# Kernel tuning notes

Measured on AMD Instinct MI355X. Metric: run time of the kernel, lower is better.

The kernel has to match this reference:

```python
import jax, jax.numpy as jnp
import numpy as np

DIM, DEPTH, HEADS, DIM_HEAD, MLP_DIM = 512, 6, 8, 64, 2048
INNER = HEADS * DIM_HEAD
EPS = 1e-5


def _layernorm(x, s, b):
    mu = jnp.mean(x, axis=-1, keepdims=True)
    var = jnp.mean(jnp.square(x - mu), axis=-1, keepdims=True)
    return (x - mu) * jax.lax.rsqrt(var + EPS) * s + b


def setup_inputs() -> dict:
    key = jax.random.key(0)
    ks = jax.random.split(key, 12)
    d = {
        "x": jax.random.normal(ks[0], (8, 1024, DIM), dtype=jnp.float32),
        "ln1_s": jnp.ones((DEPTH, DIM), jnp.float32),
        "ln1_b": jnp.zeros((DEPTH, DIM), jnp.float32),
        "w_qkv": jax.random.normal(ks[1], (DEPTH, DIM, 3 * INNER), dtype=jnp.float32) * (DIM ** -0.5),
        "w_out": jax.random.normal(ks[2], (DEPTH, INNER, DIM), dtype=jnp.float32) * (INNER ** -0.5),
        "b_out": jnp.zeros((DEPTH, DIM), jnp.float32),
        "ln2_s": jnp.ones((DEPTH, DIM), jnp.float32),
        "ln2_b": jnp.zeros((DEPTH, DIM), jnp.float32),
        "w1": jax.random.normal(ks[3], (DEPTH, DIM, MLP_DIM), dtype=jnp.float32) * (DIM ** -0.5),
        "b1": jnp.zeros((DEPTH, MLP_DIM), jnp.float32),
        "w2": jax.random.normal(ks[4], (DEPTH, MLP_DIM, DIM), dtype=jnp.float32) * (MLP_DIM ** -0.5),
        "b2": jnp.zeros((DEPTH, DIM), jnp.float32),
    }
    return d


def reference(x, ln1_s, ln1_b, w_qkv, w_out, b_out, ln2_s, ln2_b, w1, b1, w2, b2):
    b, n, _ = x.shape
    scale = DIM_HEAD ** -0.5
    for i in range(DEPTH):
        # --- PreNorm Attention with residual ---
        h = _layernorm(x, ln1_s[i], ln1_b[i])
        qkv = h @ w_qkv[i]                                  # [b, n, 3*inner]
        q, k, v = jnp.split(qkv, 3, axis=-1)
        q = q.reshape(b, n, HEADS, DIM_HEAD)
        k = k.reshape(b, n, HEADS, DIM_HEAD)
        v = v.reshape(b, n, HEADS, DIM_HEAD)
        dots = jnp.einsum('bihd,bjhd->bhij', q, k) * scale  # [b, h, n, n]
        attn = jax.nn.softmax(dots, axis=-1)
        out = jnp.einsum('bhij,bjhd->bihd', attn, v).reshape(b, n, INNER)
        x = out @ w_out[i] + b_out[i] + x
        # --- PreNorm FeedForward with residual ---
        h = _layernorm(x, ln2_s[i], ln2_b[i])
        h = jax.nn.gelu(h @ w1[i] + b1[i], approximate=False)
        x = h @ w2[i] + b2[i] + x
    return x
```

## Files before the change

kernel.cpp:

```cpp
#include <hip/hip_runtime.h>
#include <cstdint>
#include <cstddef>

#define M_TOK 8192
#define DIMM  512
#define HEADS 8
#define DH    64
#define MLPD  2048
#define DEPTH 6

typedef unsigned short u16;
typedef unsigned int   u32;
typedef __attribute__((ext_vector_type(8))) short short8;
typedef __attribute__((ext_vector_type(4))) float f32x4;

__device__ __forceinline__ float bf2f(u16 u){ return __uint_as_float(((u32)u) << 16); }
__device__ __forceinline__ u16 f2bf(float f){
    u32 x = __float_as_uint(f);
    u32 r = x + 0x7fffu + ((x >> 16) & 1u);
    return (u16)(r >> 16);
}
__device__ __forceinline__ u32 cvt_pk_bf16(float a, float b){
    u32 r;
    asm("v_cvt_pk_bf16_f32 %0, %1, %2" : "=v"(r) : "v"(a), "v"(b));
    return r;
}
__device__ __forceinline__ void async16(const u16* g, u16* l){
    __builtin_amdgcn_global_load_lds(
        (const __attribute__((address_space(1))) void*)(uintptr_t)(const void*)g,
        (__attribute__((address_space(3))) void*)(u32)(uintptr_t)(void*)l,
        16, 0, 0);
}
__device__ __forceinline__ void xcd_swizzle(int& bx, int& by){
    int nbx = gridDim.x, nby = gridDim.y;
    if ((nby & 7) == 0){
        int i = by * nbx + bx;
        int xcd = i & 7, j = i >> 3, ypg = nby >> 3;
        int yq = j / nbx;
        by = xcd * ypg + yq;
        bx = j - yq * nbx;
    }
}

__global__ void k_transpose_cvt(const float* __restrict__ in, u16* __restrict__ out, int R, int C){
    __shared__ u16 tile[32][33];
    size_t zoff = (size_t)blockIdx.z * R * C;
    in += zoff; out += zoff;
    int c0 = blockIdx.x * 32, r0 = blockIdx.y * 32;
    int tx = threadIdx.x, ty = threadIdx.y;
    #pragma unroll
    for (int i = 0; i < 32; i += 8)
        tile[ty + i][tx] = f2bf(in[(size_t)(r0 + ty + i) * C + c0 + tx]);
    __syncthreads();
    #pragma unroll
    for (int i = 0; i < 32; i += 8)
        out[(size_t)(c0 + ty + i) * R + r0 + tx] = tile[tx][ty + i];
}

__global__ __launch_bounds__(256) void k_layernorm(const float* __restrict__ x,
                                                   const float* __restrict__ s,
                                                   const float* __restrict__ b,
                                                   u16* __restrict__ out){
    int row = blockIdx.x * 4 + (threadIdx.x >> 6);
    int lane = threadIdx.x & 63;
    const float* xp = x + (size_t)row * DIMM + lane * 8;
    float v[8];
    #pragma unroll
    for (int c = 0; c < 8; c++) v[c] = xp[c];
    float sum = 0.f, sq = 0.f;
    #pragma unroll
    for (int c = 0; c < 8; c++){ sum += v[c]; sq += v[c] * v[c]; }
    #pragma unroll
    for (int m = 32; m >= 1; m >>= 1){
        sum += __shfl_xor(sum, m);
        sq  += __shfl_xor(sq,  m);
    }
    float mu  = sum * (1.f / DIMM);
    float var = sq * (1.f / DIMM) - mu * mu;
    float rs  = rsqrtf(var + 1e-5f);
    u16* op = out + (size_t)row * DIMM + lane * 8;
    #pragma unroll
    for (int c = 0; c < 8; c++){
        int col = lane * 8 + c;
        op[c] = f2bf((v[c] - mu) * rs * s[col] + b[col]);
    }
}

__device__ __forceinline__ float gelu_exact(float v){
    return 0.5f * v * (1.f + erff(v * 0.70710678118654752f));
}

#define LDT64 72

template<int MODE>
__global__ __launch_bounds__(256) void k_gemm128b(const u16* __restrict__ A,
                                                  const u16* __restrict__ Bt,
                                                  const float* __restrict__ bias,
                                                  u16* __restrict__ Cout,
                                                  int M, int N, int K){
    __shared__ u16 As[2][128 * 64];
    __shared__ u16 Bs[2][128 * 64];
    int bx = blockIdx.x, by = blockIdx.y;
    xcd_swizzle(bx, by);
    int m0 = by * 128, n0 = bx * 128;
    int t = threadIdx.x;
    int w = t >> 6, lane = t & 63;
    int mi = lane & 15, quad = lane >> 4;
    int wr = w >> 1, wc = w & 1;

    int grow = lane >> 3, gcol = (lane & 7) * 8;
    const u16* agl = A  + (size_t)(m0 + w * 32 + grow) * K + gcol;
    const u16* bgl = Bt + (size_t)(n0 + w * 32 + grow) * K + gcol;

    f32x4 acc[4][4];
    #pragma unroll
    for (int mt = 0; mt < 4; mt++)
        #pragma unroll
        for (int nt = 0; nt < 4; nt++) acc[mt][nt] = (f32x4){0.f, 0.f, 0.f, 0.f};

    int nt_k = K >> 6;
    {
        u16* asl = &As[0][(w * 32) * 64];
        u16* bsl = &Bs[0][(w * 32) * 64];
        #pragma unroll
        for (int i = 0; i < 4; i++){
            async16(agl + (size_t)(i * 8) * K, asl + i * 8 * 64);
            async16(bgl + (size_t)(i * 8) * K, bsl + i * 8 * 64);
        }
    }
    __syncthreads();

    for (int td = 0; td < nt_k; td++){
        int cur = td & 1;
        if (td + 1 < nt_k){
            int k0 = (td + 1) << 6;
            u16* asl = &As[cur ^ 1][(w * 32) * 64];
            u16* bsl = &Bs[cur ^ 1][(w * 32) * 64];
            #pragma unroll
            for (int i = 0; i < 4; i++){
                async16(agl + (size_t)(i * 8) * K + k0, asl + i * 8 * 64);
                async16(bgl + (size_t)(i * 8) * K + k0, bsl + i * 8 * 64);
            }
        }
        const u16* Ab = &As[cur][0];
        const u16* Bb = &Bs[cur][0];
        #pragma unroll
        for (int kk = 0; kk < 64; kk += 32){
            short8 af[4], bf[4];
            #pragma unroll
            for (int mt = 0; mt < 4; mt++)
                af[mt] = *(const short8*)&Ab[(wr * 64 + mt * 16 + mi) * 64 + kk + quad * 8];
            #pragma unroll
            for (int nt = 0; nt < 4; nt++)
                bf[nt] = *(const short8*)&Bb[(wc * 64 + nt * 16 + mi) * 64 + kk + quad * 8];
            #pragma unroll
            for (int mt = 0; mt < 4; mt++)
                #pragma unroll
                for (int nt = 0; nt < 4; nt++)
                    acc[mt][nt] = __builtin_amdgcn_mfma_f32_16x16x32_bf16(af[mt], bf[nt], acc[mt][nt], 0, 0, 0);
        }
        __syncthreads();
    }

    float bv[4];
    if (MODE == 1){
        #pragma unroll
        for (int nt = 0; nt < 4; nt++) bv[nt] = bias[n0 + wc * 64 + nt * 16 + mi];
    }
    u16* cs = ((u16*)As) + w * 16 * LDT64;
    int erow = lane >> 2, ecol = (lane & 3) * 16;
    #pragma unroll
    for (int mt = 0; mt < 4; mt++){
        #pragma unroll
        for (int nt = 0; nt < 4; nt++)
            #pragma unroll
            for (int r = 0; r < 4; r++){
                float v = acc[mt][nt][r];
                if (MODE == 1) v = gelu_exact(v + bv[nt]);
                cs[(quad * 4 + r) * LDT64 + nt * 16 + mi] = f2bf(v);
            }
        uint4 c0 = *(const uint4*)&cs[erow * LDT64 + ecol];
        uint4 c1 = *(const uint4*)&cs[erow * LDT64 + ecol + 8];
        u16* cp = Cout + (size_t)(m0 + wr * 64 + mt * 16 + erow) * N + n0 + wc * 64 + ecol;
        *(uint4*)cp       = c0;
        *(uint4*)(cp + 8) = c1;
    }
}

__global__ __launch_bounds__(256) void k_gemm128_res(const u16* __restrict__ A,
                                                     const u16* __restrict__ Bt,
                                                     const float* __restrict__ bias,
                                                     float* __restrict__ xres,
                                                     int M, int N, int K){
    __shared__ u16 As[2][128 * 64];
    __shared__ u16 Bs[2][128 * 64];
    int bx = blockIdx.x, by = blockIdx.y;
    xcd_swizzle(bx, by);
    int m0 = by * 128, n0 = bx * 128;
    int t = threadIdx.x;
    int w = t >> 6, lane = t & 63;
    int mi = lane & 15, quad = lane >> 4;
    int wr = w >> 1, wc = w & 1;

    int grow = lane >> 3, gcol = (lane & 7) * 8;
    const u16* agl = A  + (size_t)(m0 + w * 32 + grow) * K + gcol;
    const u16* bgl = Bt + (size_t)(n0 + w * 32 + grow) * K + gcol;

    f32x4 acc[4][4];
    #pragma unroll
    for (int mt = 0; mt < 4; mt++)
        #pragma unroll
        for (int nt = 0; nt < 4; nt++) acc[mt][nt] = (f32x4){0.f, 0.f, 0.f, 0.f};

    int nt_k = K >> 6;
    {
        u16* asl = &As[0][(w * 32) * 64];
        u16* bsl = &Bs[0][(w * 32) * 64];
        #pragma unroll
        for (int i = 0; i < 4; i++){
            async16(agl + (size_t)(i * 8) * K, asl + i * 8 * 64);
            async16(bgl + (size_t)(i * 8) * K, bsl + i * 8 * 64);
        }
    }
    __syncthreads();

    for (int td = 0; td < nt_k; td++){
        int cur = td & 1;
        if (td + 1 < nt_k){
            int k0 = (td + 1) << 6;
            u16* asl = &As[cur ^ 1][(w * 32) * 64];
            u16* bsl = &Bs[cur ^ 1][(w * 32) * 64];
            #pragma unroll
            for (int i = 0; i < 4; i++){
                async16(agl + (size_t)(i * 8) * K + k0, asl + i * 8 * 64);
                async16(bgl + (size_t)(i * 8) * K + k0, bsl + i * 8 * 64);
            }
        }
        const u16* Ab = &As[cur][0];
        const u16* Bb = &Bs[cur][0];
        #pragma unroll
        for (int kk = 0; kk < 64; kk += 32){
            short8 af[4], bf[4];
            #pragma unroll
            for (int mt = 0; mt < 4; mt++)
                af[mt] = *(const short8*)&Ab[(wr * 64 + mt * 16 + mi) * 64 + kk + quad * 8];
            #pragma unroll
            for (int nt = 0; nt < 4; nt++)
                bf[nt] = *(const short8*)&Bb[(wc * 64 + nt * 16 + mi) * 64 + kk + quad * 8];
            #pragma unroll
            for (int mt = 0; mt < 4; mt++)
                #pragma unroll
                for (int nt = 0; nt < 4; nt++)
                    acc[mt][nt] = __builtin_amdgcn_mfma_f32_16x16x32_bf16(af[mt], bf[nt], acc[mt][nt], 0, 0, 0);
        }
        __syncthreads();
    }

    float bv[4];
    #pragma unroll
    for (int nt = 0; nt < 4; nt++) bv[nt] = bias[n0 + wc * 64 + nt * 16 + mi];
    float* cs = ((float*)As) + w * 16 * LDT64;
    int erow = lane >> 2, ecol = (lane & 3) * 16;
    #pragma unroll
    for (int mt = 0; mt < 4; mt++){
        #pragma unroll
        for (int nt = 0; nt < 4; nt++)
            #pragma unroll
            for (int r = 0; r < 4; r++)
                cs[(quad * 4 + r) * LDT64 + nt * 16 + mi] = acc[mt][nt][r] + bv[nt];
        float* xp = xres + (size_t)(m0 + wr * 64 + mt * 16 + erow) * N + n0 + wc * 64 + ecol;
        #pragma unroll
        for (int j = 0; j < 4; j++){
            float4 cv = *(const float4*)&cs[erow * LDT64 + ecol + j * 4];
            float4 xv = *(const float4*)(xp + j * 4);
            xv.x += cv.x; xv.y += cv.y; xv.z += cv.z; xv.w += cv.w;
            *(float4*)(xp + j * 4) = xv;
        }
    }
}

#define LDK 72
#define C1_LOG2E 0.18033688011112042f
#define C2_LOG2E 11.541560327111707f

__global__ __launch_bounds__(256) void k_flash(const u16* __restrict__ qkv, u16* __restrict__ out){
    __shared__ u16 Ks[64 * LDK];
    __shared__ u16 Vt[80 * LDK];
    __shared__ u16 Ps[4][32 * LDK];
    int wg = (blockIdx.x & 7) * 64 + (blockIdx.x >> 3);
    int qt = wg & 7, h = (wg >> 3) & 7, b = wg >> 6;
    int t = threadIdx.x;
    int w = t >> 6, lane = t & 63;
    int mi = lane & 15, quad = lane >> 4;

    for (int i = t; i < 16 * 64; i += 256){
        int d = i >> 6, kk = i & 63;
        Vt[(64 + d) * LDK + kk] = 0x3F80;
    }

    const u16* base = qkv + ((size_t)b * 1024) * 1536;
    int hoff = h * 64;

    short8 qf[2][2];
    #pragma unroll
    for (int qh = 0; qh < 2; qh++){
        int qrow = qt * 128 + w * 32 + qh * 16 + mi;
        const u16* qp = base + (size_t)qrow * 1536 + hoff + quad * 8;
        qf[qh][0] = *(const short8*)(qp);
        qf[qh][1] = *(const short8*)(qp + 32);
    }

    f32x4 o[2][4];
    f32x4 lacc[2];
    #pragma unroll
    for (int qh = 0; qh < 2; qh++){
        #pragma unroll
        for (int nb = 0; nb < 4; nb++) o[qh][nb] = (f32x4){0.f, 0.f, 0.f, 0.f};
        lacc[qh] = (f32x4){0.f, 0.f, 0.f, 0.f};
    }

    int kkey = t >> 2, kseg = t & 3;
    const u16* kgp = base + (size_t)kkey * 1536 + 512 + hoff + kseg * 16;
    int vkey = lane, vdg = w;
    const u16* vgp = base + (size_t)vkey * 1536 + 1024 + hoff + vdg * 16;

    uint4 kv0 = *(const uint4*)(kgp);
    uint4 kv1 = *(const uint4*)(kgp + 8);
    uint4 vv0 = *(const uint4*)(vgp);
    uint4 vv1 = *(const uint4*)(vgp + 8);

    for (int kt = 0; kt < 16; kt++){
        __syncthreads();
        *(uint4*)&Ks[kkey * LDK + kseg * 16]     = kv0;
        *(uint4*)&Ks[kkey * LDK + kseg * 16 + 8] = kv1;
        u16 vtmp[16];
        *(uint4*)&vtmp[0] = vv0;
        *(uint4*)&vtmp[8] = vv1;
        #pragma unroll
        for (int i = 0; i < 16; i++)
            Vt[(vdg * 16 + i) * LDK + vkey] = vtmp[i];
        __syncthreads();

        if (kt < 15){
            size_t koff = (size_t)(kt + 1) * 64 * 1536;
            kv0 = *(const uint4*)(kgp + koff);
            kv1 = *(const uint4*)(kgp + koff + 8);
            vv0 = *(const uint4*)(vgp + koff);
            vv1 = *(const uint4*)(vgp + koff + 8);
        }

        short8 kb[4][2];
        #pragma unroll
        for (int nb = 0; nb < 4; nb++){
            kb[nb][0] = *(const short8*)&Ks[(nb * 16 + mi) * LDK + quad * 8];
            kb[nb][1] = *(const short8*)&Ks[(nb * 16 + mi) * LDK + quad * 8 + 32];
        }
        #pragma unroll
        for (int qh = 0; qh < 2; qh++){
            #pragma unroll
            for (int nb = 0; nb < 4; nb++){
                f32x4 z = (f32x4){0.f, 0.f, 0.f, 0.f};
                z = __builtin_amdgcn_mfma_f32_16x16x32_bf16(qf[qh][0], kb[nb][0], z, 0, 0, 0);
                z = __builtin_amdgcn_mfma_f32_16x16x32_bf16(qf[qh][1], kb[nb][1], z, 0, 0, 0);
                float e0 = exp2f(fmaf(z[0], C1_LOG2E, -C2_LOG2E));
                float e1 = exp2f(fmaf(z[1], C1_LOG2E, -C2_LOG2E));
                float e2 = exp2f(fmaf(z[2], C1_LOG2E, -C2_LOG2E));
                float e3 = exp2f(fmaf(z[3], C1_LOG2E, -C2_LOG2E));
                u32 p01 = cvt_pk_bf16(e0, e1);
                u32 p23 = cvt_pk_bf16(e2, e3);
                u16* pp = &Ps[w][(qh * 16 + quad * 4) * LDK + nb * 16 + mi];
                pp[0]       = (u16)p01;
                pp[LDK]     = (u16)(p01 >> 16);
                pp[2 * LDK] = (u16)p23;
                pp[3 * LDK] = (u16)(p23 >> 16);
            }
        }
        short8 vb[4][2], lb[2];
        #pragma unroll
        for (int nb = 0; nb < 4; nb++){
            vb[nb][0] = *(const short8*)&Vt[(nb * 16 + mi) * LDK + quad * 8];
            vb[nb][1] = *(const short8*)&Vt[(nb * 16 + mi) * LDK + quad * 8 + 32];
        }
        lb[0] = *(const short8*)&Vt[(64 + mi) * LDK + quad * 8];
        lb[1] = *(const short8*)&Vt[(64 + mi) * LDK + quad * 8 + 32];
        #pragma unroll
        for (int qh = 0; qh < 2; qh++){
            const short8 a0 = *(const short8*)&Ps[w][(qh * 16 + mi) * LDK + quad * 8];
            const short8 a1 = *(const short8*)&Ps[w][(qh * 16 + mi) * LDK + quad * 8 + 32];
            #pragma unroll
            for (int nb = 0; nb < 4; nb++){
                o[qh][nb] = __builtin_amdgcn_mfma_f32_16x16x32_bf16(a0, vb[nb][0], o[qh][nb], 0, 0, 0);
                o[qh][nb] = __builtin_amdgcn_mfma_f32_16x16x32_bf16(a1, vb[nb][1], o[qh][nb], 0, 0, 0);
            }
            lacc[qh] = __builtin_amdgcn_mfma_f32_16x16x32_bf16(a0, lb[0], lacc[qh], 0, 0, 0);
            lacc[qh] = __builtin_amdgcn_mfma_f32_16x16x32_bf16(a1, lb[1], lacc[qh], 0, 0, 0);
        }
    }
    #pragma unroll
    for (int qh = 0; qh < 2; qh++){
        float invl[4];
        #pragma unroll
        for (int r = 0; r < 4; r++) invl[r] = 1.f / lacc[qh][r];
        u16* op = out + ((size_t)b * 1024 + qt * 128 + w * 32 + qh * 16) * 512 + hoff;
        #pragma unroll
        for (int nb = 0; nb < 4; nb++){
            u32 c01 = cvt_pk_bf16(o[qh][nb][0] * invl[0], o[qh][nb][1] * invl[1]);
            u32 c23 = cvt_pk_bf16(o[qh][nb][2] * invl[2], o[qh][nb][3] * invl[3]);
            u16* cp = op + (size_t)(quad * 4) * 512 + nb * 16 + mi;
            cp[0]       = (u16)c01;
            cp[512]     = (u16)(c01 >> 16);
            cp[2 * 512] = (u16)c23;
            cp[3 * 512] = (u16)(c23 >> 16);
        }
    }
}

extern "C" void kernel_launch(void* const* d_in, const int* in_sizes, int n_in,
                              void* d_out, int out_size, void* d_ws, size_t ws_size,
                              hipStream_t stream){
    const float* x_in  = (const float*)d_in[0];
    const float* ln1_s = (const float*)d_in[1];
    const float* ln1_b = (const float*)d_in[2];
    const float* w_qkv = (const float*)d_in[3];
    const float* w_out = (const float*)d_in[4];
    const float* b_out = (const float*)d_in[5];
    const float* ln2_s = (const float*)d_in[6];
    const float* ln2_b = (const float*)d_in[7];
    const float* w1    = (const float*)d_in[8];
    const float* b1    = (const float*)d_in[9];
    const float* w2    = (const float*)d_in[10];
    const float* b2    = (const float*)d_in[11];
    float* out = (float*)d_out;

    char* ws = (char*)d_ws;
    float* x_f32 = (float*)ws;   ws += (size_t)M_TOK * DIMM * 4;
    u16* bufA    = (u16*)ws;     ws += (size_t)M_TOK * DIMM * 2;
    u16* bufB    = (u16*)ws;     ws += (size_t)M_TOK * MLPD * 2;
    u16* wbase   = (u16*)ws;
    size_t per_layer_w = (size_t)(1536 + 512 + 2048 + 2048) * 512;

    size_t used_big = (size_t)(ws - (char*)d_ws) + per_layer_w * 2 * DEPTH;
    bool big = (ws_size >= used_big);

    u16* ln_out   = bufA;
    u16* attn_out = bufA;
    u16* qkv      = bufB;
    u16* mlp_h    = bufB;

    size_t x_bytes = (size_t)M_TOK * DIMM * sizeof(float);
    hipMemcpyAsync(x_f32, x_in, x_bytes, hipMemcpyDeviceToDevice, stream);

    const size_t off_qkv = 0;
    const size_t off_out = (size_t)1536 * 512;
    const size_t off_w1  = off_out + (size_t)512 * 512;
    const size_t off_w2  = off_w1 + (size_t)2048 * 512;

    if (big){
        k_transpose_cvt<<<dim3(48, 16, 6), dim3(32, 8), 0, stream>>>(w_qkv, wbase + off_qkv * DEPTH, 512, 1536);
        k_transpose_cvt<<<dim3(16, 16, 6), dim3(32, 8), 0, stream>>>(w_out, wbase + off_out * DEPTH, 512, 512);
        k_transpose_cvt<<<dim3(64, 16, 6), dim3(32, 8), 0, stream>>>(w1,    wbase + off_w1  * DEPTH, 512, 2048);
        k_transpose_cvt<<<dim3(16, 64, 6), dim3(32, 8), 0, stream>>>(w2,    wbase + off_w2  * DEPTH, 2048, 512);
    }

    for (int i = 0; i < DEPTH; i++){
        u16 *wqkvT, *woutT, *w1T, *w2T;
        if (big){
            wqkvT = wbase + off_qkv * DEPTH + (size_t)i * 1536 * 512;
            woutT = wbase + off_out * DEPTH + (size_t)i * 512 * 512;
            w1T   = wbase + off_w1  * DEPTH + (size_t)i * 2048 * 512;
            w2T   = wbase + off_w2  * DEPTH + (size_t)i * 512 * 2048;
        } else {
            wqkvT = wbase + off_qkv; woutT = wbase + off_out;
            w1T   = wbase + off_w1;  w2T   = wbase + off_w2;
            k_transpose_cvt<<<dim3(48, 16), dim3(32, 8), 0, stream>>>(w_qkv + (size_t)i * 512 * 1536, wqkvT, 512, 1536);
            k_transpose_cvt<<<dim3(16, 16), dim3(32, 8), 0, stream>>>(w_out + (size_t)i * 512 * 512,  woutT, 512, 512);
            k_transpose_cvt<<<dim3(64, 16), dim3(32, 8), 0, stream>>>(w1    + (size_t)i * 512 * 2048, w1T,   512, 2048);
            k_transpose_cvt<<<dim3(16, 64), dim3(32, 8), 0, stream>>>(w2    + (size_t)i * 2048 * 512, w2T,   2048, 512);
        }

        k_layernorm<<<dim3(M_TOK / 4), dim3(256), 0, stream>>>(x_f32, ln1_s + i * 512, ln1_b + i * 512, ln_out);
        k_gemm128b<0><<<dim3(12, 64), dim3(256), 0, stream>>>(ln_out, wqkvT, nullptr, qkv,
                                                              M_TOK, 1536, 512);
        k_flash<<<dim3(512), dim3(256), 0, stream>>>(qkv, attn_out);
        k_gemm128_res<<<dim3(4, 64), dim3(256), 0, stream>>>(attn_out, woutT, b_out + i * 512, x_f32,
                                                             M_TOK, 512, 512);
        k_layernorm<<<dim3(M_TOK / 4), dim3(256), 0, stream>>>(x_f32, ln2_s + i * 512, ln2_b + i * 512, ln_out);
        k_gemm128b<1><<<dim3(16, 64), dim3(256), 0, stream>>>(ln_out, w1T, b1 + i * 2048, mlp_h,
                                                              M_TOK, 2048, 512);
        k_gemm128_res<<<dim3(4, 64), dim3(256), 0, stream>>>(mlp_h, w2T, b2 + i * 512, x_f32,
                                                             M_TOK, 512, 2048);
    }
    hipMemcpyAsync(out, x_f32, x_bytes, hipMemcpyDeviceToDevice, stream);
}
```

Baseline: 1.195 ms.

## Split attention KV range across two workgroups and add a polynomial erf approximation

The attention kernel now splits the 16 key tiles into two halves, so 1024 workgroups run instead of 512. Each half writes unnormalized fp32 partial outputs and row sums, and a new combine kernel adds the halves, normalizes and converts to bf16. This targets low occupancy, since the old 512-block grid may not fill 256 CUs well. It costs an extra kernel launch and extra fp32 partial-result memory traffic, and the workspace layout changes to make room. Separately, GELU's erff is replaced with the Abramowitz-Stegun polynomial approximation (max error about 1.5e-7), which uses a fast reciprocal and exp2 to make the MLP epilogue cheaper.

Result: faster. 1.153 ms (-3.5%).

```diff
diff --git a/kernel.cpp b/kernel.cpp
--- a/kernel.cpp
+++ b/kernel.cpp
@@ -86,8 +86,17 @@
     }
 }
 
+__device__ __forceinline__ float erf_as(float x){
+    float ax = fabsf(x);
+    float t  = __builtin_amdgcn_rcpf(fmaf(0.3275911f, ax, 1.f));
+    float y  = fmaf(fmaf(fmaf(fmaf(1.061405429f, t, -1.453152027f), t,
+                              1.421413741f), t, -0.284496736f), t, 0.254829592f) * t;
+    float e  = exp2f(-ax * ax * 1.4426950408889634f);
+    float r  = 1.f - y * e;
+    return copysignf(r, x);
+}
 __device__ __forceinline__ float gelu_exact(float v){
-    return 0.5f * v * (1.f + erff(v * 0.70710678118654752f));
+    return 0.5f * v * (1.f + erf_as(v * 0.70710678118654752f));
 }
 
 #define LDT64 72
@@ -282,13 +291,17 @@
 #define LDK 72
 #define C1_LOG2E 0.18033688011112042f
 #define C2_LOG2E 11.541560327111707f
-
-__global__ __launch_bounds__(256) void k_flash(const u16* __restrict__ qkv, u16* __restrict__ out){
+#define OSPLIT (M_TOK * 512)
+#define LSPLIT (M_TOK * 8)
+
+__global__ __launch_bounds__(256) void k_flash_split(const u16* __restrict__ qkv,
+                                                     float* __restrict__ Opart,
+                                                     float* __restrict__ lpart){
     __shared__ u16 Ks[64 * LDK];
     __shared__ u16 Vt[80 * LDK];
     __shared__ u16 Ps[4][32 * LDK];
-    int wg = (blockIdx.x & 7) * 64 + (blockIdx.x >> 3);
-    int qt = wg & 7, h = (wg >> 3) & 7, b = wg >> 6;
+    int wg = (blockIdx.x & 7) * 128 + (blockIdx.x >> 3);
+    int qt = wg & 7, h = (wg >> 3) & 7, sp = (wg >> 6) & 1, b = wg >> 7;
     int t = threadIdx.x;
     int w = t >> 6, lane = t & 63;
     int mi = lane & 15, quad = lane >> 4;
@@ -324,12 +337,14 @@
     int vkey = lane, vdg = w;
     const u16* vgp = base + (size_t)vkey * 1536 + 1024 + hoff + vdg * 16;
 
-    uint4 kv0 = *(const uint4*)(kgp);
-    uint4 kv1 = *(const uint4*)(kgp + 8);
-    uint4 vv0 = *(const uint4*)(vgp);
-    uint4 vv1 = *(const uint4*)(vgp + 8);
-
-    for (int kt = 0; kt < 16; kt++){
+    int kt0 = sp * 8;
+    size_t koff0 = (size_t)kt0 * 64 * 1536;
+    uint4 kv0 = *(const uint4*)(kgp + koff0);
+    uint4 kv1 = *(const uint4*)(kgp + koff0 + 8);
+    uint4 vv0 = *(const uint4*)(vgp + koff0);
+    uint4 vv1 = *(const uint4*)(vgp + koff0 + 8);
+
+    for (int kt = kt0; kt < kt0 + 8; kt++){
         __syncthreads();
         *(uint4*)&Ks[kkey * LDK + kseg * 16]     = kv0;
         *(uint4*)&Ks[kkey * LDK + kseg * 16 + 8] = kv1;
@@ -341,7 +356,7 @@
             Vt[(vdg * 16 + i) * LDK + vkey] = vtmp[i];
         __syncthreads();
 
-        if (kt < 15){
+        if (kt < kt0 + 7){
             size_t koff = (size_t)(kt + 1) * 64 * 1536;
             kv0 = *(const uint4*)(kgp + koff);
             kv1 = *(const uint4*)(kgp + koff + 8);
@@ -396,6 +411,153 @@
             lacc[qh] = __builtin_amdgcn_mfma_f32_16x16x32_bf16(a1, lb[1], lacc[qh], 0, 0, 0);
         }
     }
+    float* Ob = Opart + (size_t)sp * OSPLIT;
+    float* lb2 = lpart + (size_t)sp * LSPLIT;
+    #pragma unroll
+    for (int qh = 0; qh < 2; qh++){
+        int grow0 = b * 1024 + qt * 128 + w * 32 + qh * 16;
+        float* op = Ob + (size_t)grow0 * 512 + hoff;
+        #pragma unroll
+        for (int nb = 0; nb < 4; nb++)
+            #pragma unroll
+            for (int r = 0; r < 4; r++)
+                op[(size_t)(quad * 4 + r) * 512 + nb * 16 + mi] = o[qh][nb][r];
+        if (mi == 0){
+            #pragma unroll
+            for (int r = 0; r < 4; r++)
+                lb2[(size_t)(grow0 + quad * 4 + r) * 8 + h] = lacc[qh][r];
+        }
+    }
+}
+
+__global__ __launch_bounds__(256) void k_combine(const float* __restrict__ Opart,
+                                                 const float* __restrict__ lpart,
+                                                 u16* __restrict__ out){
+    int tid = blockIdx.x * 256 + threadIdx.x;
+    size_t basei = (size_t)tid * 8;
+    int row = (int)(basei >> 9), col = (int)(basei & 511), h = col >> 6;
+    float l = lpart[(size_t)row * 8 + h] + lpart[(size_t)LSPLIT + (size_t)row * 8 + h];
+    float inv = 1.f / l;
+    float4 a0 = *(const float4*)(Opart + basei);
+    float4 a1 = *(const float4*)(Opart + basei + 4);
+    float4 b0 = *(const float4*)(Opart + (size_t)OSPLIT + basei);
+    float4 b1 = *(const float4*)(Opart + (size_t)OSPLIT + basei + 4);
+    uint4 r;
+    r.x = cvt_pk_bf16((a0.x + b0.x) * inv, (a0.y + b0.y) * inv);
+    r.y = cvt_pk_bf16((a0.z + b0.z) * inv, (a0.w + b0.w) * inv);
+    r.z = cvt_pk_bf16((a1.x + b1.x) * inv, (a1.y + b1.y) * inv);
+    r.w = cvt_pk_bf16((a1.z + b1.z) * inv, (a1.w + b1.w) * inv);
+    *(uint4*)(out + basei) = r;
+}
+
+__global__ __launch_bounds__(256) void k_flash(const u16* __restrict__ qkv, u16* __restrict__ out){
+    __shared__ u16 Ks[64 * LDK];
+    __shared__ u16 Vt[80 * LDK];
+    __shared__ u16 Ps[4][32 * LDK];
+    int wg = (blockIdx.x & 7) * 64 + (blockIdx.x >> 3);
+    int qt = wg & 7, h = (wg >> 3) & 7, b = wg >> 6;
+    int t = threadIdx.x;
+    int w = t >> 6, lane = t & 63;
+    int mi = lane & 15, quad = lane >> 4;
+
+    for (int i = t; i < 16 * 64; i += 256){
+        int d = i >> 6, kk = i & 63;
+        Vt[(64 + d) * LDK + kk] = 0x3F80;
+    }
+    const u16* base = qkv + ((size_t)b * 1024) * 1536;
+    int hoff = h * 64;
+
+    short8 qf[2][2];
+    #pragma unroll
+    for (int qh = 0; qh < 2; qh++){
+        int qrow = qt * 128 + w * 32 + qh * 16 + mi;
+        const u16* qp = base + (size_t)qrow * 1536 + hoff + quad * 8;
+        qf[qh][0] = *(const short8*)(qp);
+        qf[qh][1] = *(const short8*)(qp + 32);
+    }
+    f32x4 o[2][4];
+    f32x4 lacc[2];
+    #pragma unroll
+    for (int qh = 0; qh < 2; qh++){
+        #pragma unroll
+        for (int nb = 0; nb < 4; nb++) o[qh][nb] = (f32x4){0.f, 0.f, 0.f, 0.f};
+        lacc[qh] = (f32x4){0.f, 0.f, 0.f, 0.f};
+    }
+    int kkey = t >> 2, kseg = t & 3;
+    const u16* kgp = base + (size_t)kkey * 1536 + 512 + hoff + kseg * 16;
+    int vkey = lane, vdg = w;
+    const u16* vgp = base + (size_t)vkey * 1536 + 1024 + hoff + vdg * 16;
+
+    uint4 kv0 = *(const uint4*)(kgp);
+    uint4 kv1 = *(const uint4*)(kgp + 8);
+    uint4 vv0 = *(const uint4*)(vgp);
+    uint4 vv1 = *(const uint4*)(vgp + 8);
+
+    for (int kt = 0; kt < 16; kt++){
+        __syncthreads();
+        *(uint4*)&Ks[kkey * LDK + kseg * 16]     = kv0;
+        *(uint4*)&Ks[kkey * LDK + kseg * 16 + 8] = kv1;
+        u16 vtmp[16];
+        *(uint4*)&vtmp[0] = vv0;
+        *(uint4*)&vtmp[8] = vv1;
+        #pragma unroll
+        for (int i = 0; i < 16; i++)
+            Vt[(vdg * 16 + i) * LDK + vkey] = vtmp[i];
+        __syncthreads();
+        if (kt < 15){
+            size_t koff = (size_t)(kt + 1) * 64 * 1536;
+            kv0 = *(const uint4*)(kgp + koff);
+            kv1 = *(const uint4*)(kgp + koff + 8);
+            vv0 = *(const uint4*)(vgp + koff);
+            vv1 = *(const uint4*)(vgp + koff + 8);
+        }
+        short8 kb[4][2];
+        #pragma unroll
+        for (int nb = 0; nb < 4; nb++){
+            kb[nb][0] = *(const short8*)&Ks[(nb * 16 + mi) * LDK + quad * 8];
+            kb[nb][1] = *(const short8*)&Ks[(nb * 16 + mi) * LDK + quad * 8 + 32];
+        }
+        #pragma unroll
+        for (int qh = 0; qh < 2; qh++){
+            #pragma unroll
+            for (int nb = 0; nb < 4; nb++){
+                f32x4 z = (f32x4){0.f, 0.f, 0.f, 0.f};
+                z = __builtin_amdgcn_mfma_f32_16x16x32_bf16(qf[qh][0], kb[nb][0], z, 0, 0, 0);
+                z = __builtin_amdgcn_mfma_f32_16x16x32_bf16(qf[qh][1], kb[nb][1], z, 0, 0, 0);
+                float e0 = exp2f(fmaf(z[0], C1_LOG2E, -C2_LOG2E));
+                float e1 = exp2f(fmaf(z[1], C1_LOG2E, -C2_LOG2E));
+                float e2 = exp2f(fmaf(z[2], C1_LOG2E, -C2_LOG2E));
+                float e3 = exp2f(fmaf(z[3], C1_LOG2E, -C2_LOG2E));
+                u32 p01 = cvt_pk_bf16(e0, e1);
+                u32 p23 = cvt_pk_bf16(e2, e3);
+                u16* pp = &Ps[w][(qh * 16 + quad * 4) * LDK + nb * 16 + mi];
+                pp[0]       = (u16)p01;
+                pp[LDK]     = (u16)(p01 >> 16);
+                pp[2 * LDK] = (u16)p23;
+                pp[3 * LDK] = (u16)(p23 >> 16);
+            }
+        }
+        short8 vb[4][2], lb[2];
+        #pragma unroll
+        for (int nb = 0; nb < 4; nb++){
+            vb[nb][0] = *(const short8*)&Vt[(nb * 16 + mi) * LDK + quad * 8];
+            vb[nb][1] = *(const short8*)&Vt[(nb * 16 + mi) * LDK + quad * 8 + 32];
+        }
+        lb[0] = *(const short8*)&Vt[(64 + mi) * LDK + quad * 8];
+        lb[1] = *(const short8*)&Vt[(64 + mi) * LDK + quad * 8 + 32];
+        #pragma unroll
+        for (int qh = 0; qh < 2; qh++){
+            const short8 a0 = *(const short8*)&Ps[w][(qh * 16 + mi) * LDK + quad * 8];
+            const short8 a1 = *(const short8*)&Ps[w][(qh * 16 + mi) * LDK + quad * 8 + 32];
+            #pragma unroll
+            for (int nb = 0; nb < 4; nb++){
+                o[qh][nb] = __builtin_amdgcn_mfma_f32_16x16x32_bf16(a0, vb[nb][0], o[qh][nb], 0, 0, 0);
+                o[qh][nb] = __builtin_amdgcn_mfma_f32_16x16x32_bf16(a1, vb[nb][1], o[qh][nb], 0, 0, 0);
+            }
+            lacc[qh] = __builtin_amdgcn_mfma_f32_16x16x32_bf16(a0, lb[0], lacc[qh], 0, 0, 0);
+            lacc[qh] = __builtin_amdgcn_mfma_f32_16x16x32_bf16(a1, lb[1], lacc[qh], 0, 0, 0);
+        }
+    }
     #pragma unroll
     for (int qh = 0; qh < 2; qh++){
         float invl[4];
@@ -436,11 +598,17 @@
     float* x_f32 = (float*)ws;   ws += (size_t)M_TOK * DIMM * 4;
     u16* bufA    = (u16*)ws;     ws += (size_t)M_TOK * DIMM * 2;
     u16* bufB    = (u16*)ws;     ws += (size_t)M_TOK * MLPD * 2;
-    u16* wbase   = (u16*)ws;
+
     size_t per_layer_w = (size_t)(1536 + 512 + 2048 + 2048) * 512;
-
-    size_t used_big = (size_t)(ws - (char*)d_ws) + per_layer_w * 2 * DEPTH;
-    bool big = (ws_size >= used_big);
+    size_t split_bytes = (size_t)2 * OSPLIT * 4 + (size_t)2 * LSPLIT * 4;
+    size_t base_used = (size_t)(ws - (char*)d_ws);
+
+    bool split_ok = ws_size >= base_used + split_bytes + per_layer_w * 2;
+    float* Opart = (float*)ws;
+    float* lpart = (float*)(ws + (size_t)2 * OSPLIT * 4);
+    u16* wbase = split_ok ? (u16*)(ws + split_bytes) : (u16*)ws;
+    size_t wb_off = (size_t)((char*)wbase - (char*)d_ws);
+    bool big = ws_size >= wb_off + per_layer_w * 2 * DEPTH;
 
     u16* ln_out   = bufA;
     u16* attn_out = bufA;
@@ -481,7 +649,12 @@
         k_layernorm<<<dim3(M_TOK / 4), dim3(256), 0, stream>>>(x_f32, ln1_s + i * 512, ln1_b + i * 512, ln_out);
         k_gemm128b<0><<<dim3(12, 64), dim3(256), 0, stream>>>(ln_out, wqkvT, nullptr, qkv,
                                                               M_TOK, 1536, 512);
-        k_flash<<<dim3(512), dim3(256), 0, stream>>>(qkv, attn_out);
+        if (split_ok){
+            k_flash_split<<<dim3(1024), dim3(256), 0, stream>>>(qkv, Opart, lpart);
+            k_combine<<<dim3(2048), dim3(256), 0, stream>>>(Opart, lpart, attn_out);
+        } else {
+            k_flash<<<dim3(512), dim3(256), 0, stream>>>(qkv, attn_out);
+        }
         k_gemm128_res<<<dim3(4, 64), dim3(256), 0, stream>>>(attn_out, woutT, b_out + i * 512, x_f32,
                                                              M_TOK, 512, 512);
         k_layernorm<<<dim3(M_TOK / 4), dim3(256), 0, stream>>>(x_f32, ln2_s + i * 512, ln2_b + i * 512, ln_out);
```
